# Optimization experiments

Hardware: AMD Instinct MI355X
Metric: run time of the kernel (lower is better)

## Reference

```python
import jax, jax.numpy as jnp
import numpy as np

B, E, K = 512, 4096, 1024      # batch, emb_dim, key_dim
M, L = 1024, 32                # mem_size, prompt_length
TOP_K = 4
EPS = 1e-12


def _l2norm(x, axis=-1):
    n = jnp.linalg.norm(x, axis=axis, keepdims=True)
    return x / jnp.maximum(n, EPS)


def setup_inputs() -> dict:
    key = jax.random.key(0)
    k1, k2, k3, k4 = jax.random.split(key, 4)
    return {
        "x_query": jax.random.normal(k1, (B, E), dtype=jnp.float32),
        "W_proj": jax.random.normal(k2, (K, E), dtype=jnp.float32) * 0.02,
        "prompt_memory": jax.random.normal(k3, (M, L, E), dtype=jnp.float32) * 0.02,
        "prompt_keys": jax.random.normal(k4, (M, K), dtype=jnp.float32) * 0.02,
        "top_k": TOP_K,
    }


def reference(x_query, W_proj, prompt_memory, prompt_keys, top_k):
    # x_proj = Linear(emb_dim -> key_dim, no bias): x @ W.T
    x_proj = jnp.einsum("be,ke->bk", x_query, W_proj)          # [B, K]
    x_norm = _l2norm(x_proj)                                     # [B, K]
    key_norm = _l2norm(prompt_keys)                              # [M, K]
    sim = jnp.einsum("bk,mk->bm", x_norm, key_norm)             # [B, M]
    _, idx = jax.lax.top_k(sim, top_k)                           # [B, top_k]
    sel_prompts = prompt_memory[idx]                             # [B, top_k, L, E]
    sel_keys = _l2norm(prompt_keys[idx], axis=2)                 # [B, top_k, K]
    refined = jnp.einsum("bk,btk->bt", x_norm, sel_keys)        # [B, top_k]
    w = jax.nn.softmax(refined, axis=1)                          # [B, top_k]
    # softmax-weighted sum over selected prompts
    out = jnp.einsum("btle,bt->ble", sel_prompts, w)            # [B, L, E]
    return out
```

## Files before the change

### kernel.cpp

```cpp
#include <hip/hip_runtime.h>
#include <math.h>

#define BDIM 512
#define EDIM 4096
#define KDIM 1024
#define MDIM 1024
#define LDIM 32
#define TOPK 4
#define EPSF 1e-12f

typedef __attribute__((ext_vector_type(8))) short short8;
typedef __attribute__((ext_vector_type(4))) float f32x4;

struct us4 { ushort x, y, z, w; };

__device__ inline ushort f2bf_rn(float x) {
    union { float f; unsigned u; } v; v.f = x;
    unsigned r = (v.u + 0x7FFF + ((v.u >> 16) & 1)) >> 16;
    return (ushort)r;
}
__device__ inline float bf2f(ushort h) {
    union { unsigned u; float f; } v; v.u = ((unsigned)h) << 16;
    return v.f;
}

__global__ __launch_bounds__(256)
void split_kernel(const float* __restrict__ x, ushort* __restrict__ hi,
                  ushort* __restrict__ lo, int n4)
{
    for (int i = blockIdx.x * 256 + threadIdx.x; i < n4; i += gridDim.x * 256) {
        float4 v = ((const float4*)x)[i];
        us4 h, l;
        h.x = f2bf_rn(v.x); l.x = f2bf_rn(v.x - bf2f(h.x));
        h.y = f2bf_rn(v.y); l.y = f2bf_rn(v.y - bf2f(h.y));
        h.z = f2bf_rn(v.z); l.z = f2bf_rn(v.z - bf2f(h.z));
        h.w = f2bf_rn(v.w); l.w = f2bf_rn(v.w - bf2f(h.w));
        ((us4*)hi)[i] = h;
        ((us4*)lo)[i] = l;
    }
}

__global__ __launch_bounds__(256)
void gemm_mfma_split(const ushort* __restrict__ Ah, const ushort* __restrict__ Al,
                     const ushort* __restrict__ Bh, const ushort* __restrict__ Bl,
                     float* __restrict__ Cp, int M, int N, int K, int Kchunk)
{
    __shared__ ushort lds[4][64][40];

    const int t  = threadIdx.x;
    const int bn = blockIdx.x, bm = blockIdx.y, kz = blockIdx.z;

    const int srow = t >> 2, sg = t & 3;
    const size_t aoff = (size_t)(bm * 64 + srow) * K + sg * 8 + (size_t)kz * Kchunk;
    const size_t boff = (size_t)(bn * 64 + srow) * K + sg * 8 + (size_t)kz * Kchunk;

    const int lane = t & 63, wid = t >> 6;
    const int wr = wid >> 1, wc = wid & 1;
    const int fr = lane & 15, fg = lane >> 4;

    f32x4 acc[2][2];
    #pragma unroll
    for (int i = 0; i < 2; ++i)
        #pragma unroll
        for (int j = 0; j < 2; ++j)
            acc[i][j] = (f32x4){0.f, 0.f, 0.f, 0.f};

    for (int k0 = 0; k0 < Kchunk; k0 += 32) {
        *(short8*)(&lds[0][srow][sg * 8]) = *(const short8*)(Ah + aoff + k0);
        *(short8*)(&lds[1][srow][sg * 8]) = *(const short8*)(Al + aoff + k0);
        *(short8*)(&lds[2][srow][sg * 8]) = *(const short8*)(Bh + boff + k0);
        *(short8*)(&lds[3][srow][sg * 8]) = *(const short8*)(Bl + boff + k0);
        __syncthreads();

        short8 ah[2], al[2], bh[2], bl[2];
        #pragma unroll
        for (int i = 0; i < 2; ++i) {
            ah[i] = *(const short8*)(&lds[0][wr * 32 + i * 16 + fr][fg * 8]);
            al[i] = *(const short8*)(&lds[1][wr * 32 + i * 16 + fr][fg * 8]);
            bh[i] = *(const short8*)(&lds[2][wc * 32 + i * 16 + fr][fg * 8]);
            bl[i] = *(const short8*)(&lds[3][wc * 32 + i * 16 + fr][fg * 8]);
        }
        #pragma unroll
        for (int i = 0; i < 2; ++i)
            #pragma unroll
            for (int j = 0; j < 2; ++j) {
                acc[i][j] = __builtin_amdgcn_mfma_f32_16x16x32_bf16(ah[i], bh[j], acc[i][j], 0, 0, 0);
                acc[i][j] = __builtin_amdgcn_mfma_f32_16x16x32_bf16(ah[i], bl[j], acc[i][j], 0, 0, 0);
                acc[i][j] = __builtin_amdgcn_mfma_f32_16x16x32_bf16(al[i], bh[j], acc[i][j], 0, 0, 0);
            }
        __syncthreads();
    }

    float* Cz = Cp + (size_t)kz * M * N;
    #pragma unroll
    for (int i = 0; i < 2; ++i)
        #pragma unroll
        for (int j = 0; j < 2; ++j)
            #pragma unroll
            for (int q = 0; q < 4; ++q) {
                int orow = bm * 64 + wr * 32 + i * 16 + (lane >> 4) * 4 + q;
                int ocol = bn * 64 + wc * 32 + j * 16 + (lane & 15);
                Cz[(size_t)orow * N + ocol] = acc[i][j][q];
            }
}

__global__ __launch_bounds__(256)
void reduce4_kernel(const float* __restrict__ Cp, float* __restrict__ out,
                    int n4, int nsplit)
{
    int i = blockIdx.x * 256 + threadIdx.x;
    if (i >= n4) return;
    float4 s = ((const float4*)Cp)[i];
    for (int z = 1; z < nsplit; ++z) {
        float4 v = ((const float4*)Cp)[(size_t)z * n4 + i];
        s.x += v.x; s.y += v.y; s.z += v.z; s.w += v.w;
    }
    ((float4*)out)[i] = s;
}

__global__ __launch_bounds__(256)
void reduce_scale_kernel(const float* __restrict__ Cp, const float* __restrict__ xn,
                         const float* __restrict__ kn, float* __restrict__ sim, int n4)
{
    int i = blockIdx.x * 256 + threadIdx.x;
    if (i >= n4) return;
    float4 s = ((const float4*)Cp)[i];
    float4 v = ((const float4*)Cp)[(size_t)n4 + i];
    s.x += v.x; s.y += v.y; s.z += v.z; s.w += v.w;
    const int b  = i >> 8;
    const int m0 = (i * 4) & 1023;
    const float sb = 1.f / fmaxf(xn[b], EPSF);
    s.x = s.x * sb / fmaxf(kn[m0 + 0], EPSF);
    s.y = s.y * sb / fmaxf(kn[m0 + 1], EPSF);
    s.z = s.z * sb / fmaxf(kn[m0 + 2], EPSF);
    s.w = s.w * sb / fmaxf(kn[m0 + 3], EPSF);
    ((float4*)sim)[i] = s;
}

__global__ __launch_bounds__(256)
void rownorm_kernel(const float* __restrict__ X, float* __restrict__ out, int ncols)
{
    const int row = blockIdx.x;
    const float* p = X + (size_t)row * ncols;
    float s = 0.f;
    for (int c = threadIdx.x * 4; c < ncols; c += 256 * 4) {
        float4 v = *(const float4*)(p + c);
        s += v.x * v.x + v.y * v.y + v.z * v.z + v.w * v.w;
    }
    #pragma unroll
    for (int off = 32; off > 0; off >>= 1) s += __shfl_down(s, off, 64);
    __shared__ float wsum[4];
    const int lane = threadIdx.x & 63, wwid = threadIdx.x >> 6;
    if (lane == 0) wsum[wwid] = s;
    __syncthreads();
    if (threadIdx.x == 0)
        out[row] = sqrtf(wsum[0] + wsum[1] + wsum[2] + wsum[3]);
}

__device__ inline bool tk_better(float x, int ix, float y, int iy) {
    return (x > y) || (x == y && ix < iy);
}
__device__ inline void tk_insert(float (&v)[4], int (&id)[4], float x, int m) {
    if (tk_better(x, m, v[3], id[3])) {
        v[3] = x; id[3] = m;
        if (tk_better(v[3], id[3], v[2], id[2])) {
            float tv = v[2]; int ti = id[2]; v[2] = v[3]; id[2] = id[3]; v[3] = tv; id[3] = ti;
            if (tk_better(v[2], id[2], v[1], id[1])) {
                tv = v[1]; ti = id[1]; v[1] = v[2]; id[1] = id[2]; v[2] = tv; id[2] = ti;
                if (tk_better(v[1], id[1], v[0], id[0])) {
                    tv = v[0]; ti = id[0]; v[0] = v[1]; id[0] = id[1]; v[1] = tv; id[1] = ti;
                }
            }
        }
    }
}
__global__ __launch_bounds__(64)
void topk_kernel(const float* __restrict__ sim, int* __restrict__ topi,
                 float* __restrict__ topv)
{
    const int b = blockIdx.x;
    const int lane = threadIdx.x;
    const float* row = sim + (size_t)b * MDIM;
    float v[4] = {-INFINITY, -INFINITY, -INFINITY, -INFINITY};
    int id[4] = {-1, -1, -1, -1};
    for (int j = 0; j < MDIM / 64; ++j) {
        int m = j * 64 + lane;
        tk_insert(v, id, row[m], m);
    }
    for (int off = 32; off >= 1; off >>= 1) {
        float pv[4]; int pi[4];
        #pragma unroll
        for (int q = 0; q < 4; ++q) {
            pv[q] = __shfl_xor(v[q], off, 64);
            pi[q] = __shfl_xor(id[q], off, 64);
        }
        #pragma unroll
        for (int q = 0; q < 4; ++q) tk_insert(v, id, pv[q], pi[q]);
    }
    if (lane == 0) {
        #pragma unroll
        for (int q = 0; q < 4; ++q) { topv[b * 4 + q] = v[q]; topi[b * 4 + q] = id[q]; }
    }
}

__global__ __launch_bounds__(256)
void gather_out_kernel(const float* __restrict__ pm, const int* __restrict__ topi,
                       const float* __restrict__ topv, float* __restrict__ out)
{
    const int bl = blockIdx.x;
    const int b = bl / LDIM, l = bl % LDIM;

    const int j0 = topi[b * 4 + 0], j1 = topi[b * 4 + 1], j2 = topi[b * 4 + 2], j3 = topi[b * 4 + 3];
    const float r0 = topv[b * 4 + 0], r1 = topv[b * 4 + 1], r2 = topv[b * 4 + 2], r3 = topv[b * 4 + 3];
    const float mx = fmaxf(fmaxf(r0, r1), fmaxf(r2, r3));
    const float e0 = expf(r0 - mx), e1 = expf(r1 - mx), e2 = expf(r2 - mx), e3 = expf(r3 - mx);
    const float inv = 1.f / (e0 + e1 + e2 + e3);
    const float w0 = e0 * inv, w1 = e1 * inv, w2 = e2 * inv, w3 = e3 * inv;

    const float4* p0 = (const float4*)(pm + ((size_t)j0 * LDIM + l) * EDIM);
    const float4* p1 = (const float4*)(pm + ((size_t)j1 * LDIM + l) * EDIM);
    const float4* p2 = (const float4*)(pm + ((size_t)j2 * LDIM + l) * EDIM);
    const float4* p3 = (const float4*)(pm + ((size_t)j3 * LDIM + l) * EDIM);
    float4* o = (float4*)(out + ((size_t)b * LDIM + l) * EDIM);

    for (int c = threadIdx.x; c < EDIM / 4; c += 256) {
        float4 a = p0[c], bb = p1[c], cc = p2[c], dd = p3[c];
        float4 r;
        r.x = w0 * a.x + w1 * bb.x + w2 * cc.x + w3 * dd.x;
        r.y = w0 * a.y + w1 * bb.y + w2 * cc.y + w3 * dd.y;
        r.z = w0 * a.z + w1 * bb.z + w2 * cc.z + w3 * dd.z;
        r.w = w0 * a.w + w1 * bb.w + w2 * cc.w + w3 * dd.w;
        o[c] = r;
    }
}

extern "C" void kernel_launch(void* const* d_in, const int* in_sizes, int n_in,
                              void* d_out, int out_size, void* d_ws, size_t ws_size,
                              hipStream_t stream)
{
    const float* x_query = (const float*)d_in[0];
    const float* W_proj  = (const float*)d_in[1];
    const float* pm      = (const float*)d_in[2];
    const float* pkeys   = (const float*)d_in[3];
    float* out = (float*)d_out;

    char* w = (char*)d_ws;
    ushort* xq_h = (ushort*)w; w += (size_t)BDIM * EDIM * 2;
    ushort* xq_l = (ushort*)w; w += (size_t)BDIM * EDIM * 2;
    ushort* wp_h = (ushort*)w; w += (size_t)KDIM * EDIM * 2;
    ushort* wp_l = (ushort*)w; w += (size_t)KDIM * EDIM * 2;
    ushort* pk_h = (ushort*)w; w += (size_t)MDIM * KDIM * 2;
    ushort* pk_l = (ushort*)w; w += (size_t)MDIM * KDIM * 2;
    ushort* xp_h = (ushort*)w; w += (size_t)BDIM * KDIM * 2;
    ushort* xp_l = (ushort*)w; w += (size_t)BDIM * KDIM * 2;
    float* Cp1    = (float*)w; w += (size_t)4 * BDIM * KDIM * 4;
    float* Cp2    = (float*)w; w += (size_t)2 * BDIM * MDIM * 4;
    float* x_proj = (float*)w; w += (size_t)BDIM * KDIM * 4;
    float* sim    = (float*)w; w += (size_t)BDIM * MDIM * 4;
    float* xn     = (float*)w; w += BDIM * 4;
    float* kn     = (float*)w; w += MDIM * 4;
    float* topv   = (float*)w; w += BDIM * TOPK * 4;
    int*   topi   = (int*)w;   w += BDIM * TOPK * 4;

    split_kernel<<<2048, 256, 0, stream>>>(x_query, xq_h, xq_l, BDIM * EDIM / 4);
    split_kernel<<<2048, 256, 0, stream>>>(W_proj, wp_h, wp_l, KDIM * EDIM / 4);
    split_kernel<<<1024, 256, 0, stream>>>(pkeys, pk_h, pk_l, MDIM * KDIM / 4);
    rownorm_kernel<<<MDIM, 256, 0, stream>>>(pkeys, kn, KDIM);

    gemm_mfma_split<<<dim3(KDIM / 64, BDIM / 64, 4), 256, 0, stream>>>(
        xq_h, xq_l, wp_h, wp_l, Cp1, BDIM, KDIM, EDIM, EDIM / 4);
    reduce4_kernel<<<BDIM * KDIM / 4 / 256, 256, 0, stream>>>(Cp1, x_proj, BDIM * KDIM / 4, 4);

    rownorm_kernel<<<BDIM, 256, 0, stream>>>(x_proj, xn, KDIM);
    split_kernel<<<512, 256, 0, stream>>>(x_proj, xp_h, xp_l, BDIM * KDIM / 4);

    gemm_mfma_split<<<dim3(MDIM / 64, BDIM / 64, 2), 256, 0, stream>>>(
        xp_h, xp_l, pk_h, pk_l, Cp2, BDIM, MDIM, KDIM, KDIM / 2);
    reduce_scale_kernel<<<BDIM * MDIM / 4 / 256, 256, 0, stream>>>(
        Cp2, xn, kn, sim, BDIM * MDIM / 4);

    topk_kernel<<<BDIM, 64, 0, stream>>>(sim, topi, topv);

    gather_out_kernel<<<BDIM * LDIM, 256, 0, stream>>>(pm, topi, topv, out);
}
```

Baseline: 271.3 us.

## Fuse split launches and reduce/norm/split stages; reorder gather with nontemporal stores

Merges the three bf16 hi/lo split launches into one kernel that picks its source by block range. Fuses the split-K reduction, the row L2 norm and the hi/lo split of x_proj into one kernel, so the fp32 x_proj buffer is never written and re-read. Changes the gather block mapping so consecutive blocks take different batch rows at the same prompt position, and writes the output with nontemporal stores. This cuts launches and memory traffic, but the fused norm now sums in a different order and the new gather order may change cache locality.

```diff
diff --git a/kernel.cpp b/kernel.cpp
--- a/kernel.cpp
+++ b/kernel.cpp
@@ -25,11 +25,22 @@
 }
 
 __global__ __launch_bounds__(256)
-void split_kernel(const float* __restrict__ x, ushort* __restrict__ hi,
-                  ushort* __restrict__ lo, int n4)
-{
-    for (int i = blockIdx.x * 256 + threadIdx.x; i < n4; i += gridDim.x * 256) {
-        float4 v = ((const float4*)x)[i];
+void split_all_kernel(const float* __restrict__ xq, const float* __restrict__ wp,
+                      const float* __restrict__ pk,
+                      ushort* __restrict__ xq_h, ushort* __restrict__ xq_l,
+                      ushort* __restrict__ wp_h, ushort* __restrict__ wp_l,
+                      ushort* __restrict__ pk_h, ushort* __restrict__ pk_l)
+{
+    const int blk = blockIdx.x;
+    const float* src; ushort* hi; ushort* lo; int base;
+    if (blk < 512)       { src = xq; hi = xq_h; lo = xq_l; base = blk * 1024; }
+    else if (blk < 1536) { src = wp; hi = wp_h; lo = wp_l; base = (blk - 512) * 1024; }
+    else                 { src = pk; hi = pk_h; lo = pk_l; base = (blk - 1536) * 1024; }
+
+    #pragma unroll
+    for (int it = 0; it < 4; ++it) {
+        const int i = base + it * 256 + threadIdx.x;
+        float4 v = ((const float4*)src)[i];
         us4 h, l;
         h.x = f2bf_rn(v.x); l.x = f2bf_rn(v.x - bf2f(h.x));
         h.y = f2bf_rn(v.y); l.y = f2bf_rn(v.y - bf2f(h.y));
@@ -105,17 +116,38 @@
 }
 
 __global__ __launch_bounds__(256)
-void reduce4_kernel(const float* __restrict__ Cp, float* __restrict__ out,
-                    int n4, int nsplit)
-{
-    int i = blockIdx.x * 256 + threadIdx.x;
-    if (i >= n4) return;
+void reduce_split_norm_kernel(const float* __restrict__ Cp,
+                              ushort* __restrict__ xh, ushort* __restrict__ xl,
+                              float* __restrict__ xn)
+{
+    const int b = blockIdx.x;
+    const int i = b * 256 + threadIdx.x;
+    const int n4 = BDIM * KDIM / 4;
+
     float4 s = ((const float4*)Cp)[i];
-    for (int z = 1; z < nsplit; ++z) {
+    #pragma unroll
+    for (int z = 1; z < 4; ++z) {
         float4 v = ((const float4*)Cp)[(size_t)z * n4 + i];
         s.x += v.x; s.y += v.y; s.z += v.z; s.w += v.w;
     }
-    ((float4*)out)[i] = s;
+
+    us4 h, l;
+    h.x = f2bf_rn(s.x); l.x = f2bf_rn(s.x - bf2f(h.x));
+    h.y = f2bf_rn(s.y); l.y = f2bf_rn(s.y - bf2f(h.y));
+    h.z = f2bf_rn(s.z); l.z = f2bf_rn(s.z - bf2f(h.z));
+    h.w = f2bf_rn(s.w); l.w = f2bf_rn(s.w - bf2f(h.w));
+    ((us4*)xh)[i] = h;
+    ((us4*)xl)[i] = l;
+
+    float sq = s.x * s.x + s.y * s.y + s.z * s.z + s.w * s.w;
+    #pragma unroll
+    for (int off = 32; off > 0; off >>= 1) sq += __shfl_down(sq, off, 64);
+    __shared__ float wsum[4];
+    const int lane = threadIdx.x & 63, wwid = threadIdx.x >> 6;
+    if (lane == 0) wsum[wwid] = sq;
+    __syncthreads();
+    if (threadIdx.x == 0)
+        xn[b] = sqrtf(wsum[0] + wsum[1] + wsum[2] + wsum[3]);
 }
 
 __global__ __launch_bounds__(256)
@@ -208,7 +240,8 @@
                        const float* __restrict__ topv, float* __restrict__ out)
 {
     const int bl = blockIdx.x;
-    const int b = bl / LDIM, l = bl % LDIM;
+    const int b = bl & (BDIM - 1);
+    const int l = bl >> 9;
 
     const int j0 = topi[b * 4 + 0], j1 = topi[b * 4 + 1], j2 = topi[b * 4 + 2], j3 = topi[b * 4 + 3];
     const float r0 = topv[b * 4 + 0], r1 = topv[b * 4 + 1], r2 = topv[b * 4 + 2], r3 = topv[b * 4 + 3];
@@ -217,20 +250,16 @@
     const float inv = 1.f / (e0 + e1 + e2 + e3);
     const float w0 = e0 * inv, w1 = e1 * inv, w2 = e2 * inv, w3 = e3 * inv;
 
-    const float4* p0 = (const float4*)(pm + ((size_t)j0 * LDIM + l) * EDIM);
-    const float4* p1 = (const float4*)(pm + ((size_t)j1 * LDIM + l) * EDIM);
-    const float4* p2 = (const float4*)(pm + ((size_t)j2 * LDIM + l) * EDIM);
-    const float4* p3 = (const float4*)(pm + ((size_t)j3 * LDIM + l) * EDIM);
-    float4* o = (float4*)(out + ((size_t)b * LDIM + l) * EDIM);
+    const f32x4* p0 = (const f32x4*)(pm + ((size_t)j0 * LDIM + l) * EDIM);
+    const f32x4* p1 = (const f32x4*)(pm + ((size_t)j1 * LDIM + l) * EDIM);
+    const f32x4* p2 = (const f32x4*)(pm + ((size_t)j2 * LDIM + l) * EDIM);
+    const f32x4* p3 = (const f32x4*)(pm + ((size_t)j3 * LDIM + l) * EDIM);
+    f32x4* o = (f32x4*)(out + ((size_t)b * LDIM + l) * EDIM);
 
     for (int c = threadIdx.x; c < EDIM / 4; c += 256) {
-        float4 a = p0[c], bb = p1[c], cc = p2[c], dd = p3[c];
-        float4 r;
-        r.x = w0 * a.x + w1 * bb.x + w2 * cc.x + w3 * dd.x;
-        r.y = w0 * a.y + w1 * bb.y + w2 * cc.y + w3 * dd.y;
-        r.z = w0 * a.z + w1 * bb.z + w2 * cc.z + w3 * dd.z;
-        r.w = w0 * a.w + w1 * bb.w + w2 * cc.w + w3 * dd.w;
-        o[c] = r;
+        f32x4 a = p0[c], bb = p1[c], cc = p2[c], dd = p3[c];
+        f32x4 r = w0 * a + w1 * bb + w2 * cc + w3 * dd;
+        __builtin_nontemporal_store(r, &o[c]);
     }
 }
 
@@ -255,24 +284,20 @@
     ushort* xp_l = (ushort*)w; w += (size_t)BDIM * KDIM * 2;
     float* Cp1    = (float*)w; w += (size_t)4 * BDIM * KDIM * 4;
     float* Cp2    = (float*)w; w += (size_t)2 * BDIM * MDIM * 4;
-    float* x_proj = (float*)w; w += (size_t)BDIM * KDIM * 4;
     float* sim    = (float*)w; w += (size_t)BDIM * MDIM * 4;
     float* xn     = (float*)w; w += BDIM * 4;
     float* kn     = (float*)w; w += MDIM * 4;
     float* topv   = (float*)w; w += BDIM * TOPK * 4;
     int*   topi   = (int*)w;   w += BDIM * TOPK * 4;
 
-    split_kernel<<<2048, 256, 0, stream>>>(x_query, xq_h, xq_l, BDIM * EDIM / 4);
-    split_kernel<<<2048, 256, 0, stream>>>(W_proj, wp_h, wp_l, KDIM * EDIM / 4);
-    split_kernel<<<1024, 256, 0, stream>>>(pkeys, pk_h, pk_l, MDIM * KDIM / 4);
+    split_all_kernel<<<1792, 256, 0, stream>>>(
+        x_query, W_proj, pkeys, xq_h, xq_l, wp_h, wp_l, pk_h, pk_l);
     rownorm_kernel<<<MDIM, 256, 0, stream>>>(pkeys, kn, KDIM);
 
     gemm_mfma_split<<<dim3(KDIM / 64, BDIM / 64, 4), 256, 0, stream>>>(
         xq_h, xq_l, wp_h, wp_l, Cp1, BDIM, KDIM, EDIM, EDIM / 4);
-    reduce4_kernel<<<BDIM * KDIM / 4 / 256, 256, 0, stream>>>(Cp1, x_proj, BDIM * KDIM / 4, 4);
-
-    rownorm_kernel<<<BDIM, 256, 0, stream>>>(x_proj, xn, KDIM);
-    split_kernel<<<512, 256, 0, stream>>>(x_proj, xp_h, xp_l, BDIM * KDIM / 4);
+
+    reduce_split_norm_kernel<<<BDIM, 256, 0, stream>>>(Cp1, xp_h, xp_l, xn);
 
     gemm_mfma_split<<<dim3(MDIM / 64, BDIM / 64, 2), 256, 0, stream>>>(
         xp_h, xp_l, pk_h, pk_l, Cp2, BDIM, MDIM, KDIM, KDIM / 2);
```

New measurement: 241.3 us. 1.12x faster.
